# Optimization experiments

Hardware: AMD Instinct MI355X
Metric: run time of the kernel (lower is better)

## Reference

```python
import jax, jax.numpy as jnp
import numpy as np

B, S, SE = 4, 1024, 1024
E, H, M = 768, 12, 100
D = E // H
EPS = 1e-5
GELU_C = 0.7978845608028654  # sqrt(2/pi)


def _ln(x, g, b):
    mu = x.mean(-1, keepdims=True)
    v = ((x - mu) ** 2).mean(-1, keepdims=True)
    return g * (x - mu) / jnp.sqrt(v + EPS) + b


def _gelu(x):
    return 0.5 * x * (1.0 + jnp.tanh(GELU_C * (x + 0.044715 * x ** 3)))


def _split(x):  # [b,s,E] -> [b,H,s,D]
    b, s, _ = x.shape
    return x.reshape(b, s, H, D).transpose(0, 2, 1, 3)


def _merge(x):  # [b,H,s,D] -> [b,s,E]
    b, h, s, d = x.shape
    return x.transpose(0, 2, 1, 3).reshape(b, s, h * d)


def _forward(x, encoder_features, ln1_g, ln1_b, ln2_g, ln2_b,
             c_attn_w, c_attn_b, attn_proj_w, attn_proj_b,
             memory_features, mem_attn_w, mem_attn_b, mem_alpha_w, mem_alpha_b,
             fcq_w, fcq_b, fck_w, fck_b, fcv_w, fcv_b, enc_proj_w, enc_proj_b,
             fc_alpha1_w, fc_alpha1_b, fc_alpha2_w, fc_alpha2_b,
             mlp_fc_w, mlp_fc_b, mlp_proj_w, mlp_proj_b, mask_encoder):
    # ---- memory-augmented self-attention (note: original has NO 1/sqrt(d) scaling here) ----
    h = _ln(x, ln1_g, ln1_b)
    qkv = h @ c_attn_w + c_attn_b
    q, k, v = jnp.split(qkv, 3, axis=-1)
    q, k, v = _split(q), _split(k), _split(v)
    w = jax.nn.softmax(jnp.einsum('bhqd,bhkd->bhqk', q, k), axis=-1)
    a = _merge(jnp.einsum('bhqk,bhkd->bhqd', w, v))
    # memory slots are batch-independent -> compute once, broadcast over batch
    mem = memory_features[0] @ mem_attn_w + mem_attn_b  # [M, 2E]
    mk, mv = jnp.split(mem, 2, axis=-1)
    mk = mk.reshape(M, H, D).transpose(1, 2, 0)  # [H,D,M]
    mv = mv.reshape(M, H, D).transpose(1, 0, 2)  # [H,M,D]
    wm = jax.nn.softmax(jnp.einsum('bhqd,hdm->bhqm', q, mk), axis=-1)
    a1 = _merge(jnp.einsum('bhqm,hmd->bhqd', wm, mv))
    al = jax.nn.sigmoid(jnp.concatenate([a, a1], -1) @ mem_alpha_w + mem_alpha_b)
    a = al * a + (1.0 - al) * a1
    a = a @ attn_proj_w + attn_proj_b
    a = x + a  # residual (dropout = identity in eval)

    # ---- two cross-attentions sharing weights and ln_1 ----
    ha = _ln(a, ln1_g, ln1_b)

    def enc_dec(enc):
        qe = _split(ha @ fcq_w + fcq_b)
        ke = _split(enc @ fck_w + fck_b)
        ve = _split(enc @ fcv_w + fcv_b)
        we = jnp.einsum('bhqd,bhkd->bhqk', qe, ke) / np.float32(np.sqrt(D))
        we = jnp.where(mask_encoder, jnp.float32(-10000.0), we)
        we = jax.nn.softmax(we, axis=-1)
        o = _merge(jnp.einsum('bhqk,bhkd->bhqd', we, ve))
        return o @ enc_proj_w + enc_proj_b

    e1 = enc_dec(_ln(encoder_features[:, 0], ln1_g, ln1_b))
    e2 = enc_dec(_ln(encoder_features[:, 1], ln1_g, ln1_b))
    al1 = jax.nn.sigmoid(jnp.concatenate([a, e1], -1) @ fc_alpha1_w + fc_alpha1_b)
    al2 = jax.nn.sigmoid(jnp.concatenate([a, e2], -1) @ fc_alpha2_w + fc_alpha2_b)
    e1 = al1 * a + (1.0 - al1) * e1
    e2 = al2 * a + (1.0 - al2) * e2
    a = (e1 + e2) / np.float32(np.sqrt(2.0))

    # ---- MLP ----
    hm = _ln(a, ln2_g, ln2_b)
    m = _gelu(hm @ mlp_fc_w + mlp_fc_b) @ mlp_proj_w + mlp_proj_b
    return a + m


def setup_inputs() -> dict:
    key = jax.random.key(0)
    ks = iter(jax.random.split(key, 48))

    def rn(shape, s=0.02):
        return jax.random.normal(next(ks), shape, jnp.float32) * s

    return dict(
        x=jax.random.normal(next(ks), (B, S, E), jnp.float32),
        encoder_features=jax.random.normal(next(ks), (B, 2, SE, E), jnp.float32),
        mask_encoder=jax.random.bernoulli(next(ks), 0.1, (B, 1, 1, SE)),
        ln1_g=jnp.ones(E, jnp.float32), ln1_b=jnp.zeros(E, jnp.float32),
        ln2_g=jnp.ones(E, jnp.float32), ln2_b=jnp.zeros(E, jnp.float32),
        c_attn_w=rn((E, 3 * E)), c_attn_b=jnp.zeros(3 * E, jnp.float32),
        attn_proj_w=rn((E, E)), attn_proj_b=jnp.zeros(E, jnp.float32),
        memory_features=rn((1, M, E), 1.0),
        mem_attn_w=rn((E, 2 * E)), mem_attn_b=jnp.zeros(2 * E, jnp.float32),
        mem_alpha_w=rn((2 * E, E)), mem_alpha_b=jnp.zeros(E, jnp.float32),
        fcq_w=rn((E, E)), fcq_b=jnp.zeros(E, jnp.float32),
        fck_w=rn((E, E)), fck_b=jnp.zeros(E, jnp.float32),
        fcv_w=rn((E, E)), fcv_b=jnp.zeros(E, jnp.float32),
        enc_proj_w=rn((E, E)), enc_proj_b=jnp.zeros(E, jnp.float32),
        fc_alpha1_w=rn((2 * E, E)), fc_alpha1_b=jnp.zeros(E, jnp.float32),
        fc_alpha2_w=rn((2 * E, E)), fc_alpha2_b=jnp.zeros(E, jnp.float32),
        mlp_fc_w=rn((E, 4 * E)), mlp_fc_b=jnp.zeros(4 * E, jnp.float32),
        mlp_proj_w=rn((4 * E, E)), mlp_proj_b=jnp.zeros(E, jnp.float32),
    )


def reference(x, encoder_features, mask_encoder, ln1_g, ln1_b, ln2_g, ln2_b,
              c_attn_w, c_attn_b, attn_proj_w, attn_proj_b,
              memory_features, mem_attn_w, mem_attn_b, mem_alpha_w, mem_alpha_b,
              fcq_w, fcq_b, fck_w, fck_b, fcv_w, fcv_b, enc_proj_w, enc_proj_b,
              fc_alpha1_w, fc_alpha1_b, fc_alpha2_w, fc_alpha2_b,
              mlp_fc_w, mlp_fc_b, mlp_proj_w, mlp_proj_b):
    return _forward(x, encoder_features, ln1_g, ln1_b, ln2_g, ln2_b,
                    c_attn_w, c_attn_b, attn_proj_w, attn_proj_b,
                    memory_features, mem_attn_w, mem_attn_b, mem_alpha_w, mem_alpha_b,
                    fcq_w, fcq_b, fck_w, fck_b, fcv_w, fcv_b, enc_proj_w, enc_proj_b,
                    fc_alpha1_w, fc_alpha1_b, fc_alpha2_w, fc_alpha2_b,
                    mlp_fc_w, mlp_fc_b, mlp_proj_w, mlp_proj_b, mask_encoder)
```

## Files before the change

kernel.cpp:

```cpp
#include <hip/hip_runtime.h>

typedef __bf16 bf16_t;
typedef __bf16 bf16x8v __attribute__((ext_vector_type(8)));
typedef float f32x4 __attribute__((ext_vector_type(4)));

#define CB 4
#define CE 768
#define CH 12
#define CD 64

__device__ __forceinline__ float fexp2(float x) { return __builtin_amdgcn_exp2f(x); }

__device__ __forceinline__ void gload16(const void* g, void* l) {
    __builtin_amdgcn_global_load_lds((const __attribute__((address_space(1))) void*)g,
                                     (__attribute__((address_space(3))) void*)l, 16, 0, 0);
}

__device__ __forceinline__ void xcd_remap(int& bx, int& by, int gx, int gy) {
    int nwg = gx * gy;
    if ((nwg & 7) == 0) {
        int lin = by * gx + bx;
        int lin2 = (lin & 7) * (nwg >> 3) + (lin >> 3);
        bx = lin2 % gx;
        by = lin2 / gx;
    }
}

template<int BM, int BN, int CONCAT, int ACT, int RES, int OUT, int CMODE>
__global__ __launch_bounds__(256)
void gemm_n(const bf16_t* __restrict__ A0, const bf16_t* __restrict__ A1,
            const bf16_t* __restrict__ Bt, const float* __restrict__ bias,
            const float* __restrict__ bias2, const void* __restrict__ resid,
            void* __restrict__ C, void* __restrict__ C2, void* __restrict__ C3,
            int M, int N, int K, int lda, int ldc)
{
    constexpr int WM = BM / 2, WN = BN / 2, RM = WM / 16, RN = WN / 16;
    __shared__ __align__(16) bf16_t As0[BM * 64], As1[BM * 64];
    __shared__ __align__(16) bf16_t Bs0[BN * 64], Bs1[BN * 64];

    const int t = threadIdx.x;
    const int lane = t & 63, wave = t >> 6;
    int bx = blockIdx.x, by = blockIdx.y;
    xcd_remap(bx, by, gridDim.x, gridDim.y);
    const int m0 = by * BM, n0 = bx * BN;
    const int wm = (wave & 1) * WM, wn = (wave >> 1) * WN;
    const int fr = lane & 15, quad = lane >> 4;

    const int lr = lane >> 3;
    const int kof = ((lane & 7) ^ lr) * 8;

    const bf16_t* A1b = A1;
    if (CMODE == 6) A1b = A1 + (n0 >= 768 ? (long)4096 * 768 : 0);

    f32x4 acc[RM][RN];
#pragma unroll
    for (int i = 0; i < RM; i++)
#pragma unroll
        for (int j = 0; j < RN; j++)
#pragma unroll
            for (int p = 0; p < 4; p++) acc[i][j][p] = 0.f;

    auto stage = [&](bf16_t* As, bf16_t* Bs, int kt) {
        const bf16_t* Ab = A0;
        int kk = kt;
        if (CONCAT && kt >= 768) { Ab = A1b; kk = kt - 768; }
        const bf16_t* asrc = Ab + (long)(m0 + wave * 8 + lr) * lda + kk + kof;
#pragma unroll
        for (int c = 0; c < BM / 32; ++c)
            gload16(asrc + (long)c * 32 * lda, &As[(c * 32 + wave * 8) * 64]);
        const bf16_t* bsrc = Bt + (long)(n0 + wave * 8 + lr) * K + kt + kof;
#pragma unroll
        for (int c = 0; c < BN / 32; ++c)
            gload16(bsrc + (long)c * 32 * K, &Bs[(c * 32 + wave * 8) * 64]);
    };

    const int sw = fr & 7;
    auto compute = [&](const bf16_t* As, const bf16_t* Bs) {
        bf16x8v af[RM][2], bfr[RN][2];
        const int s0 = quad ^ sw;
#pragma unroll
        for (int i = 0; i < RM; ++i) {
            const char* rb = (const char*)As + (wm + i * 16 + fr) * 128;
            af[i][0] = *(const bf16x8v*)(rb + (s0 << 4));
            af[i][1] = *(const bf16x8v*)(rb + ((s0 ^ 4) << 4));
        }
#pragma unroll
        for (int j = 0; j < RN; ++j) {
            const char* rb = (const char*)Bs + (wn + j * 16 + fr) * 128;
            bfr[j][0] = *(const bf16x8v*)(rb + (s0 << 4));
            bfr[j][1] = *(const bf16x8v*)(rb + ((s0 ^ 4) << 4));
        }
#pragma unroll
        for (int ks = 0; ks < 2; ++ks)
#pragma unroll
            for (int i = 0; i < RM; ++i)
#pragma unroll
                for (int j = 0; j < RN; ++j)
                    acc[i][j] = __builtin_amdgcn_mfma_f32_16x16x32_bf16(af[i][ks], bfr[j][ks], acc[i][j], 0, 0, 0);
    };

    const int nk = K >> 6;
    stage(As0, Bs0, 0);
    __syncthreads();
    for (int kt = 0; kt + 2 <= nk; kt += 2) {
        stage(As1, Bs1, (kt + 1) << 6);
        compute(As0, Bs0);
        __syncthreads();
        if (kt + 2 < nk) stage(As0, Bs0, (kt + 2) << 6);
        compute(As1, Bs1);
        __syncthreads();
    }

    const int rq = quad * 4, cn = fr;
#pragma unroll
    for (int i = 0; i < RM; i++)
#pragma unroll
        for (int j = 0; j < RN; j++) {
            int col = n0 + wn + j * 16 + cn;
            int t3 = (CMODE == 4 || CMODE == 5) ? (col / 768) : 0;
            int cc = col - t3 * 768;
            float bv = 0.f;
            if (CMODE == 5)      bv = t3 ? bias2[cc] : bias[cc];
            else if (CMODE == 6) bv = (col < 768) ? bias[col] : bias2[col - 768];
            else if (bias)       bv = bias[col];
            const int row0 = m0 + wm + i * 16 + rq;
            float vv[4];
#pragma unroll
            for (int p = 0; p < 4; p++) {
                float v = acc[i][j][p] + bv;
                if (ACT == 1) v = 1.f / (1.f + __expf(-v));
                if (ACT == 2) {
                    float u2 = 1.5957691216057308f * (v + 0.044715f * v * v * v);
                    v = v / (1.f + __expf(-u2));
                }
                if (RES == 2) v += ((const float*)resid)[(long)(row0 + p) * ldc + col];
                vv[p] = v;
            }
            if (CMODE == 0) {
#pragma unroll
                for (int p = 0; p < 4; p++) {
                    long idx = (long)(row0 + p) * ldc + col;
                    if (OUT == 0)      ((bf16_t*)C)[idx] = (bf16_t)vv[p];
                    else if (OUT == 1) ((float*)C)[idx] = vv[p];
                    else { ((float*)C)[idx] = vv[p]; ((bf16_t*)C2)[idx] = (bf16_t)vv[p]; }
                }
            } else if (CMODE == 6) {
                long base = (col < 768) ? 0 : ((long)4096 * 768 - 768);
#pragma unroll
                for (int p = 0; p < 4; p++)
                    ((bf16_t*)C)[base + (long)(row0 + p) * 768 + col] = (bf16_t)vv[p];
            } else if (CMODE == 7) {
#pragma unroll
                for (int p = 0; p < 4; p++) {
                    long idx = (long)(row0 + p) * ldc + col;
                    float a  = (float)((const bf16_t*)C2)[idx];
                    float a1 = (float)((const bf16_t*)C3)[idx];
                    ((bf16_t*)C)[idx] = (bf16_t)(vv[p] * a + (1.f - vv[p]) * a1);
                }
            } else {
                int bb = row0 >> 10, ss0 = row0 & 1023;
                int hh = cc >> 6, dd = cc & 63;
                long srow = (long)(bb * CH + hh) * 1024 + ss0;
                long tbase = (((long)(bb * CH + hh) * 64) + dd) * 1024 + ss0;
                union { ushort4 u4; bf16_t b[4]; } pk;
#pragma unroll
                for (int p = 0; p < 4; p++) pk.b[p] = (bf16_t)vv[p];
                if (CMODE == 2) {
#pragma unroll
                    for (int p = 0; p < 4; p++)
                        ((bf16_t*)C)[(srow + p) * 64 + dd] = pk.b[p];
                } else if (CMODE == 5) {
                    if (t3 == 0) {
#pragma unroll
                        for (int p = 0; p < 4; p++)
                            ((bf16_t*)C)[(srow + p) * 64 + dd] = pk.b[p];
                    } else {
                        *(ushort4*)((bf16_t*)C2 + tbase) = pk.u4;
                    }
                } else {
                    if (t3 == 0) {
#pragma unroll
                        for (int p = 0; p < 4; p++)
                            ((bf16_t*)C)[(srow + p) * 64 + dd] = pk.b[p];
                    } else if (t3 == 1) {
#pragma unroll
                        for (int p = 0; p < 4; p++)
                            ((bf16_t*)C2)[(srow + p) * 64 + dd] = pk.b[p];
                    } else {
                        *(ushort4*)((bf16_t*)C3 + tbase) = pk.u4;
                    }
                }
            }
        }
}

template<int MODE, int QR>
__global__ __launch_bounds__(256)
void flash_attn(const bf16_t* __restrict__ Q, const bf16_t* __restrict__ K,
                const bf16_t* __restrict__ V, const int* __restrict__ mask,
                bf16_t* __restrict__ O)
{
    constexpr int QG = QR / 64;
    __shared__ __align__(16) bf16_t Qs[QR * 64];
    __shared__ __align__(16) bf16_t Ks0[64 * 64], Ks1[64 * 64];
    __shared__ __align__(16) bf16_t Vs[64 * 64];

    const int t = threadIdx.x;
    const int lane = t & 63, wave = t >> 6;
    int bx = blockIdx.x, bz = blockIdx.z;
    {
        int nwg = gridDim.x * gridDim.z;
        if ((nwg & 7) == 0) {
            int lin = bz * gridDim.x + bx;
            int lin2 = (lin & 7) * (nwg >> 3) + (lin >> 3);
            bx = lin2 % gridDim.x;
            bz = lin2 / gridDim.x;
        }
    }
    const int zq = (MODE == 1) ? (bz % 48) : bz;
    const int b = zq / CH, h = bz % CH;
    const long eoff = (MODE == 1) ? (long)(bz / 48) * ((long)4096 * 768) : 0;
    const int q0 = bx * QR;

    const bf16_t* Qb = Q + (long)zq * 65536 + (long)q0 * 64;
    const bf16_t* Kb = (MODE == 2) ? K + (long)h * (128 * 64) : K + (long)bz * 65536;
    const bf16_t* Vb = (MODE == 2) ? V + (long)h * (64 * 128) : V + (long)bz * 65536;
    const int ldv = (MODE == 2) ? 128 : 1024;
    const int NT = (MODE == 2) ? 2 : 16;
    constexpr float SCL = (MODE == 1) ? 0.18033688011112042f : 1.4426950408889634f;

    const int lr = lane >> 3, kof = ((lane & 7) ^ lr) * 8;

    auto stageK = [&](bf16_t* Ks, int kt) {
#pragma unroll
        for (int c = 0; c < 2; ++c) {
            int r = wave * 8 + c * 32;
            gload16(Kb + (long)(kt * 64 + r + lr) * 64 + kof, &Ks[r * 64]);
        }
    };
    auto stageV = [&](int kt) {
#pragma unroll
        for (int c = 0; c < 2; ++c) {
            int r = wave * 8 + c * 32;
            gload16(Vb + (long)(r + lr) * ldv + kt * 64 + kof, &Vs[r * 64]);
        }
    };

    stageK(Ks0, 0);
#pragma unroll
    for (int c = 0; c < QR / 32; ++c) {
        int r = wave * 8 + c * 32;
        gload16(Qb + (long)(r + lr) * 64 + kof, &Qs[r * 64]);
    }
    __syncthreads();

    const int fr = lane & 15, quad = lane >> 4;
    const int sw = fr & 7;
    bf16x8v qf[QG][2];
#pragma unroll
    for (int g = 0; g < QG; g++)
#pragma unroll
        for (int ks = 0; ks < 2; ks++) {
            const char* rb = (const char*)Qs + (wave * (16 * QG) + g * 16 + fr) * 128;
            bf16x8v raw = *(const bf16x8v*)(rb + (((quad ^ sw) ^ (ks << 2)) << 4));
#pragma unroll
            for (int i = 0; i < 8; i++) qf[g][ks][i] = (bf16_t)((float)raw[i] * SCL);
        }

    bf16_t* Ps = &Qs[wave * (16 * QG) * 64];

    f32x4 o[4][QG];
    float mrow[QG], lrow[QG];
#pragma unroll
    for (int g = 0; g < QG; g++) { mrow[g] = -1e30f; lrow[g] = 0.f; }
#pragma unroll
    for (int j = 0; j < 4; j++)
#pragma unroll
        for (int g = 0; g < QG; g++)
#pragma unroll
            for (int p = 0; p < 4; p++) o[j][g][p] = 0.f;

    auto qkt_sm = [&](const bf16_t* Ks, int kt) {
        f32x4 s[4][QG];
#pragma unroll
        for (int j = 0; j < 4; j++)
#pragma unroll
            for (int g = 0; g < QG; g++)
#pragma unroll
                for (int p = 0; p < 4; p++) s[j][g][p] = 0.f;
        __builtin_amdgcn_s_setprio(1);
#pragma unroll
        for (int ks = 0; ks < 2; ks++) {
            bf16x8v bk[4];
#pragma unroll
            for (int j = 0; j < 4; j++) {
                const char* rb = (const char*)Ks + (j * 16 + fr) * 128;
                bk[j] = *(const bf16x8v*)(rb + (((quad ^ sw) ^ (ks << 2)) << 4));
            }
#pragma unroll
            for (int j = 0; j < 4; j++)
#pragma unroll
                for (int g = 0; g < QG; g++)
                    s[j][g] = __builtin_amdgcn_mfma_f32_16x16x32_bf16(bk[j], qf[g][ks], s[j][g], 0, 0, 0);
        }
        __builtin_amdgcn_s_setprio(0);
        if (MODE == 1) {
#pragma unroll
            for (int j = 0; j < 4; j++) {
                int4 mv = *(const int4*)&mask[(long)b * 1024 + kt * 64 + j * 16 + quad * 4];
#pragma unroll
                for (int g = 0; g < QG; g++) {
                    s[j][g][0] = mv.x ? -14426.95f : s[j][g][0];
                    s[j][g][1] = mv.y ? -14426.95f : s[j][g][1];
                    s[j][g][2] = mv.z ? -14426.95f : s[j][g][2];
                    s[j][g][3] = mv.w ? -14426.95f : s[j][g][3];
                }
            }
        }
        if (MODE == 2) {
#pragma unroll
            for (int j = 0; j < 4; j++)
#pragma unroll
                for (int p = 0; p < 4; p++)
                    if (kt * 64 + j * 16 + quad * 4 + p >= 100)
#pragma unroll
                        for (int g = 0; g < QG; g++) s[j][g][p] = -1e30f;
        }
        float tmax[QG];
        bool need = false;
#pragma unroll
        for (int g = 0; g < QG; g++) {
            float tm = s[0][g][0];
#pragma unroll
            for (int j = 0; j < 4; j++)
#pragma unroll
                for (int p = 0; p < 4; p++) tm = fmaxf(tm, s[j][g][p]);
            tm = fmaxf(tm, __shfl_xor(tm, 16, 64));
            tm = fmaxf(tm, __shfl_xor(tm, 32, 64));
            tmax[g] = tm;
            need = need || (tm > mrow[g] + 8.f);
        }
        if (__any(need ? 1 : 0)) {
#pragma unroll
            for (int g = 0; g < QG; g++) {
                float mnew = fmaxf(mrow[g], tmax[g]);
                float alpha = fexp2(mrow[g] - mnew);
                lrow[g] *= alpha;
                mrow[g] = mnew;
                float arow[4];
#pragma unroll
                for (int p = 0; p < 4; p++)
                    arow[p] = __shfl(alpha, (lane & 48) | (quad * 4 + p), 64);
#pragma unroll
                for (int j = 0; j < 4; j++)
#pragma unroll
                    for (int p = 0; p < 4; p++) o[j][g][p] *= arow[p];
            }
        }
#pragma unroll
        for (int g = 0; g < QG; g++) {
            float rs = 0.f;
#pragma unroll
            for (int j = 0; j < 4; j++)
#pragma unroll
                for (int p = 0; p < 4; p++) {
                    float e = fexp2(s[j][g][p] - mrow[g]);
                    s[j][g][p] = e;
                    rs += e;
                }
            rs += __shfl_xor(rs, 16, 64);
            rs += __shfl_xor(rs, 32, 64);
            lrow[g] += rs;
        }
#pragma unroll
        for (int j = 0; j < 4; j++)
#pragma unroll
            for (int g = 0; g < QG; g++) {
                union { uint2 u; bf16_t bb[4]; } pk;
#pragma unroll
                for (int p = 0; p < 4; p++) pk.bb[p] = (bf16_t)s[j][g][p];
                int row = g * 16 + fr;
                *(uint2*)((char*)Ps + row * 128 +
                          (((j * 2 + (quad >> 1)) ^ sw) << 4) + ((quad & 1) << 3)) = pk.u;
            }
    };

    auto pv = [&]() {
        __builtin_amdgcn_s_setprio(1);
#pragma unroll
        for (int ks = 0; ks < 2; ks++) {
            bf16x8v af[QG], bv[4];
#pragma unroll
            for (int g = 0; g < QG; g++) {
                const char* rb = (const char*)Ps + (g * 16 + fr) * 128;
                af[g] = *(const bf16x8v*)(rb + (((quad ^ sw) ^ (ks << 2)) << 4));
            }
#pragma unroll
            for (int j = 0; j < 4; j++) {
                const char* rb = (const char*)Vs + (j * 16 + fr) * 128;
                bv[j] = *(const bf16x8v*)(rb + (((quad ^ sw) ^ (ks << 2)) << 4));
            }
#pragma unroll
            for (int j = 0; j < 4; j++)
#pragma unroll
                for (int g = 0; g < QG; g++)
                    o[j][g] = __builtin_amdgcn_mfma_f32_16x16x32_bf16(af[g], bv[j], o[j][g], 0, 0, 0);
        }
        __builtin_amdgcn_s_setprio(0);
    };

    for (int kt = 0; kt < NT; kt += 2) {
        stageV(kt);
        if (kt + 1 < NT) stageK(Ks1, kt + 1);
        qkt_sm(Ks0, kt);
        __syncthreads();
        pv();
        __syncthreads();
        stageV(kt + 1);
        if (kt + 2 < NT) stageK(Ks0, kt + 2);
        qkt_sm(Ks1, kt + 1);
        __syncthreads();
        pv();
        __syncthreads();
    }
#pragma unroll
    for (int g = 0; g < QG; g++) {
        float linv[4];
#pragma unroll
        for (int p = 0; p < 4; p++)
            linv[p] = 1.f / __shfl(lrow[g], (lane & 48) | (quad * 4 + p), 64);
#pragma unroll
        for (int p = 0; p < 4; p++) {
            int srow = q0 + wave * (16 * QG) + g * 16 + quad * 4 + p;
            long base = ((long)b * 1024 + srow) * 768 + h * 64 + eoff;
#pragma unroll
            for (int j = 0; j < 4; j++)
                O[base + j * 16 + fr] = (bf16_t)(o[j][g][p] * linv[p]);
        }
    }
}

__device__ __forceinline__ void ln_body(const float* in, bf16_t* out,
                                        const float* g, const float* b,
                                        long base, long ob, int t)
{
    __shared__ float red[4];
    float v0 = in[base + t], v1 = in[base + t + 256], v2 = in[base + t + 512];
    float s = v0 + v1 + v2;
    for (int m = 32; m; m >>= 1) s += __shfl_xor(s, m, 64);
    if ((t & 63) == 0) red[t >> 6] = s;
    __syncthreads();
    s = red[0] + red[1] + red[2] + red[3];
    __syncthreads();
    const float mu = s * (1.f / 768.f);
    float d0 = v0 - mu, d1 = v1 - mu, d2 = v2 - mu;
    float q = d0 * d0 + d1 * d1 + d2 * d2;
    for (int m = 32; m; m >>= 1) q += __shfl_xor(q, m, 64);
    if ((t & 63) == 0) red[t >> 6] = q;
    __syncthreads();
    q = red[0] + red[1] + red[2] + red[3];
    const float rstd = rsqrtf(q * (1.f / 768.f) + 1e-5f);
    out[ob + t]       = (bf16_t)(g[t]       * d0 * rstd + b[t]);
    out[ob + t + 256] = (bf16_t)(g[t + 256] * d1 * rstd + b[t + 256]);
    out[ob + t + 512] = (bf16_t)(g[t + 512] * d2 * rstd + b[t + 512]);
}

__global__ __launch_bounds__(256)
void ln_kernel(const float* __restrict__ in, bf16_t* __restrict__ out,
               const float* __restrict__ g, const float* __restrict__ b)
{
    const int r = blockIdx.x;
    ln_body(in, out, g, b, (long)r * CE, (long)r * CE, threadIdx.x);
}

__global__ __launch_bounds__(256)
void ln_enc(const float* __restrict__ encf, bf16_t* __restrict__ out,
            const float* __restrict__ g, const float* __restrict__ b)
{
    const int r = blockIdx.x;
    const int e = r >> 12, rr = r & 4095, bb = rr >> 10, s = rr & 1023;
    ln_body(encf, out, g, b, ((long)(bb * 2 + e) * 1024 + s) * CE, (long)r * CE, threadIdx.x);
}

__global__ void fuse_gates2(const bf16_t* __restrict__ gal, const bf16_t* __restrict__ eo,
                            float* __restrict__ rf)
{
    const long SZel = (long)4096 * 768;
    long idx = (long)blockIdx.x * 256 + threadIdx.x;
    float g1 = (float)gal[idx], g2 = (float)gal[idx + SZel];
    float e1 = (float)eo[idx],  e2 = (float)eo[idx + SZel];
    float r = rf[idx];
    float v = g1 * r + (1.f - g1) * e1 + g2 * r + (1.f - g2) * e2;
    rf[idx] = v * 0.7071067811865476f;
}

__global__ void zero_out(float* __restrict__ out)
{
    out[blockIdx.x * 256 + threadIdx.x] = 0.f;
}

__global__ void transpose_cast(const float* __restrict__ in, bf16_t* __restrict__ out,
                               int K, int N)
{
    __shared__ bf16_t tile[32][33];
    int n0 = blockIdx.x * 32, k0 = blockIdx.y * 32;
    int tx = threadIdx.x, ty = threadIdx.y;
    for (int i = ty; i < 32; i += 8)
        tile[i][tx] = (bf16_t)in[(long)(k0 + i) * N + n0 + tx];
    __syncthreads();
    for (int i = ty; i < 32; i += 8)
        out[(long)(n0 + i) * K + k0 + tx] = tile[tx][i];
}

__global__ void cast_pad_mem(const float* __restrict__ memf, bf16_t* __restrict__ out)
{
    int idx = blockIdx.x * 256 + threadIdx.x;
    int row = idx / 768;
    out[idx] = (row < 100) ? (bf16_t)memf[idx] : (bf16_t)0.f;
}

__global__ void repack_mem(const bf16_t* __restrict__ mem, bf16_t* __restrict__ mkt,
                           bf16_t* __restrict__ mvt)
{
    int idx = blockIdx.x * 256 + threadIdx.x;
    int d = idx & 63;
    int slot = (idx >> 6) & 127;
    int h = idx >> 13;
    bf16_t kv = (slot < 100) ? mem[slot * 1536 + h * CD + d] : (bf16_t)0.f;
    bf16_t vv = (slot < 100) ? mem[slot * 1536 + CE + h * CD + d] : (bf16_t)0.f;
    mkt[idx] = kv;
    mvt[((long)h * 64 + d) * 128 + slot] = vv;
}

extern "C" void kernel_launch(void* const* d_in, const int* in_sizes, int n_in,
                              void* d_out, int out_size, void* d_ws, size_t ws_size,
                              hipStream_t stream)
{
    (void)in_sizes; (void)n_in; (void)out_size;
    const float* x        = (const float*)d_in[0];
    const float* encf     = (const float*)d_in[1];
    const int*   maskenc  = (const int*)d_in[2];
    const float* ln1_g    = (const float*)d_in[3];
    const float* ln1_b    = (const float*)d_in[4];
    const float* ln2_g    = (const float*)d_in[5];
    const float* ln2_b    = (const float*)d_in[6];
    const float* c_attn_w = (const float*)d_in[7];
    const float* c_attn_b = (const float*)d_in[8];
    const float* aproj_w  = (const float*)d_in[9];
    const float* aproj_b  = (const float*)d_in[10];
    const float* memf     = (const float*)d_in[11];
    const float* mattn_w  = (const float*)d_in[12];
    const float* mattn_b  = (const float*)d_in[13];
    const float* malpha_w = (const float*)d_in[14];
    const float* malpha_b = (const float*)d_in[15];
    const float* fcq_w    = (const float*)d_in[16];
    const float* fcq_b    = (const float*)d_in[17];
    const float* fck_w    = (const float*)d_in[18];
    const float* fck_b    = (const float*)d_in[19];
    const float* fcv_w    = (const float*)d_in[20];
    const float* fcv_b    = (const float*)d_in[21];
    const float* eproj_w  = (const float*)d_in[22];
    const float* eproj_b  = (const float*)d_in[23];
    const float* fa1_w    = (const float*)d_in[24];
    const float* fa1_b    = (const float*)d_in[25];
    const float* fa2_w    = (const float*)d_in[26];
    const float* fa2_b    = (const float*)d_in[27];
    const float* mfc_w    = (const float*)d_in[28];
    const float* mfc_b    = (const float*)d_in[29];
    const float* mproj_w  = (const float*)d_in[30];
    const float* mproj_b  = (const float*)d_in[31];
    float* dout = (float*)d_out;

    size_t off = 0;
    auto alloc = [&](size_t bytes) -> void* {
        void* p = (char*)d_ws + off;
        off = (off + bytes + 255) & ~(size_t)255;
        return p;
    };
    const size_t SZ = (size_t)4096 * 768 * 2;
    const long SZel = (long)4096 * 768;
    bf16_t* wt_cattn  = (bf16_t*)alloc((size_t)2304 * 768 * 2);
    bf16_t* wt_aproj  = (bf16_t*)alloc((size_t)768 * 768 * 2);
    bf16_t* wt_malpha = (bf16_t*)alloc((size_t)768 * 1536 * 2);
    bf16_t* wt_fcq    = (bf16_t*)alloc((size_t)768 * 768 * 2);
    bf16_t* wt_fck    = (bf16_t*)alloc((size_t)768 * 768 * 2);
    bf16_t* wt_fcv    = (bf16_t*)alloc((size_t)768 * 768 * 2);
    bf16_t* wt_eproj  = (bf16_t*)alloc((size_t)768 * 768 * 2);
    bf16_t* wt_fa1    = (bf16_t*)alloc((size_t)768 * 1536 * 2);
    bf16_t* wt_fa2    = (bf16_t*)alloc((size_t)768 * 1536 * 2);
    bf16_t* wt_mfc    = (bf16_t*)alloc((size_t)3072 * 768 * 2);
    bf16_t* wt_mproj  = (bf16_t*)alloc((size_t)768 * 3072 * 2);
    bf16_t* wt_mattn  = (bf16_t*)alloc((size_t)1536 * 768 * 2);
    bf16_t* memb   = (bf16_t*)alloc((size_t)128 * 768 * 2);
    bf16_t* membuf = (bf16_t*)alloc((size_t)128 * 1536 * 2);
    bf16_t* mkt    = (bf16_t*)alloc((size_t)CH * 128 * 64 * 2);
    bf16_t* mvt    = (bf16_t*)alloc((size_t)CH * 64 * 128 * 2);
    bf16_t* bufA   = (bf16_t*)alloc(SZ);
    bf16_t* qbuf   = (bf16_t*)alloc(SZ);
    bf16_t* kbuf   = (bf16_t*)alloc(2 * SZ);
    bf16_t* vtbuf  = (bf16_t*)alloc(2 * SZ);
    bf16_t* asbuf  = (bf16_t*)alloc(2 * SZ);
    bf16_t* bufB   = (bf16_t*)alloc(2 * SZ);
    float*  residf = (float*)alloc((size_t)4096 * 768 * 4);
    bf16_t* residb = (bf16_t*)alloc(SZ);

    if (off > ws_size) {
        zero_out<<<12288, 256, 0, stream>>>(dout);
        return;
    }
    bf16_t* mid = kbuf;
    bf16_t* galbuf = kbuf;
    bf16_t* eobuf = bufB;

    const dim3 blk(256);

    auto T = [&](const float* w, bf16_t* wt, int Kd, int Nd) {
        transpose_cast<<<dim3(Nd / 32, Kd / 32), dim3(32, 8), 0, stream>>>(w, wt, Kd, Nd);
    };
    T(c_attn_w, wt_cattn, 768, 2304);
    T(aproj_w, wt_aproj, 768, 768);
    T(malpha_w, wt_malpha, 1536, 768);
    T(fcq_w, wt_fcq, 768, 768);
    T(fck_w, wt_fck, 768, 768);
    T(fcv_w, wt_fcv, 768, 768);
    T(eproj_w, wt_eproj, 768, 768);
    T(fa1_w, wt_fa1, 1536, 768);
    T(fa2_w, wt_fa2, 1536, 768);
    T(mfc_w, wt_mfc, 768, 3072);
    T(mproj_w, wt_mproj, 3072, 768);
    T(mattn_w, wt_mattn, 768, 1536);

    cast_pad_mem<<<384, blk, 0, stream>>>(memf, memb);
    gemm_n<64,64,0,0,0,0,0><<<dim3(24, 2), blk, 0, stream>>>(
        memb, nullptr, wt_mattn, mattn_b, nullptr, nullptr, membuf, nullptr, nullptr,
        128, 1536, 768, 768, 1536);
    repack_mem<<<384, blk, 0, stream>>>(membuf, mkt, mvt);

    ln_kernel<<<4096, blk, 0, stream>>>(x, bufA, ln1_g, ln1_b);
    gemm_n<128,128,0,0,0,0,4><<<dim3(18, 32), blk, 0, stream>>>(
        bufA, nullptr, wt_cattn, c_attn_b, nullptr, nullptr, qbuf, kbuf, vtbuf,
        4096, 2304, 768, 768, 0);

    flash_attn<0,64><<<dim3(16, 1, 48), blk, 0, stream>>>(qbuf, kbuf, vtbuf, nullptr, asbuf);
    flash_attn<2,64><<<dim3(16, 1, 48), blk, 0, stream>>>(qbuf, mkt, mvt, nullptr, asbuf + SZel);

    gemm_n<128,64,1,1,0,0,7><<<dim3(12, 32), blk, 0, stream>>>(
        asbuf, asbuf + SZel, wt_malpha, malpha_b, nullptr, nullptr, bufA, asbuf, asbuf + SZel,
        4096, 768, 1536, 768, 768);
    gemm_n<128,64,0,0,2,2,0><<<dim3(12, 32), blk, 0, stream>>>(
        bufA, nullptr, wt_aproj, aproj_b, nullptr, x, residf, residb, nullptr,
        4096, 768, 768, 768, 768);

    ln_kernel<<<4096, blk, 0, stream>>>(residf, bufA, ln1_g, ln1_b);
    gemm_n<128,64,0,0,0,0,2><<<dim3(12, 32), blk, 0, stream>>>(
        bufA, nullptr, wt_fcq, fcq_b, nullptr, nullptr, qbuf, nullptr, nullptr,
        4096, 768, 768, 768, 0);

    ln_enc<<<8192, blk, 0, stream>>>(encf, bufB, ln1_g, ln1_b);
    gemm_n<128,128,0,0,0,0,5><<<dim3(12, 64), blk, 0, stream>>>(
        bufB, nullptr, wt_fck, fck_b, fcv_b, nullptr, kbuf, vtbuf, nullptr,
        8192, 1536, 768, 768, 0);
    flash_attn<1,128><<<dim3(8, 1, 96), blk, 0, stream>>>(
        qbuf, kbuf, vtbuf, maskenc, asbuf);
    gemm_n<128,128,0,0,0,0,0><<<dim3(6, 64), blk, 0, stream>>>(
        asbuf, nullptr, wt_eproj, eproj_b, nullptr, nullptr, eobuf, nullptr, nullptr,
        8192, 768, 768, 768, 768);
    gemm_n<128,64,1,1,0,0,6><<<dim3(24, 32), blk, 0, stream>>>(
        residb, eobuf, wt_fa1, fa1_b, fa2_b, nullptr, galbuf, nullptr, nullptr,
        4096, 1536, 1536, 768, 768);
    fuse_gates2<<<12288, blk, 0, stream>>>(galbuf, eobuf, residf);

    ln_kernel<<<4096, blk, 0, stream>>>(residf, bufA, ln2_g, ln2_b);
    gemm_n<128,128,0,2,0,0,0><<<dim3(24, 32), blk, 0, stream>>>(
        bufA, nullptr, wt_mfc, mfc_b, nullptr, nullptr, mid, nullptr, nullptr,
        4096, 3072, 768, 768, 3072);
    gemm_n<128,64,0,0,2,1,0><<<dim3(12, 32), blk, 0, stream>>>(
        mid, nullptr, wt_mproj, mproj_b, nullptr, residf, dout, nullptr, nullptr,
        4096, 768, 3072, 3072, 768);
}
```

Before: 593.4 us.

## Batch weight transposes into one launch and shrink GEMM tiles for more workgroups

All twelve weight transpose-casts now run in a single kernel launch. Each block finds its weight matrix through a prefix-sum table passed as a kernel argument. Separately, several GEMMs move from 128x128 or 128x64 tiles to 128x64 or 64x64 tiles with matching grids, so more workgroups cover the 256 CUs of the MI355X. This trades more total operand reloads and less reuse per tile for better load balance and less launch overhead.

```diff
diff --git a/kernel.cpp b/kernel.cpp
--- a/kernel.cpp
+++ b/kernel.cpp
@@ -499,11 +499,27 @@
     out[blockIdx.x * 256 + threadIdx.x] = 0.f;
 }
 
-__global__ void transpose_cast(const float* __restrict__ in, bf16_t* __restrict__ out,
-                               int K, int N)
+#define NTW 12
+struct TTab {
+    const float* src[NTW];
+    unsigned long dst[NTW];
+    int kn[NTW];
+    int pre[NTW + 1];
+};
+
+__global__ void transpose_all(TTab tt, char* __restrict__ ws)
 {
     __shared__ bf16_t tile[32][33];
-    int n0 = blockIdx.x * 32, k0 = blockIdx.y * 32;
+    int tb = blockIdx.x;
+    int e = 0;
+#pragma unroll
+    for (int i = 0; i < NTW; i++) if (tb >= tt.pre[i + 1]) e = i + 1;
+    int local = tb - tt.pre[e];
+    const int K = tt.kn[e] >> 16, N = tt.kn[e] & 0xffff;
+    const float* in = tt.src[e];
+    bf16_t* out = (bf16_t*)(ws + tt.dst[e]);
+    const int ntx = N / 32;
+    const int n0 = (local % ntx) * 32, k0 = (local / ntx) * 32;
     int tx = threadIdx.x, ty = threadIdx.y;
     for (int i = ty; i < 32; i += 8)
         tile[i][tx] = (bf16_t)in[(long)(k0 + i) * N + n0 + tx];
@@ -614,21 +630,25 @@
 
     const dim3 blk(256);
 
-    auto T = [&](const float* w, bf16_t* wt, int Kd, int Nd) {
-        transpose_cast<<<dim3(Nd / 32, Kd / 32), dim3(32, 8), 0, stream>>>(w, wt, Kd, Nd);
-    };
-    T(c_attn_w, wt_cattn, 768, 2304);
-    T(aproj_w, wt_aproj, 768, 768);
-    T(malpha_w, wt_malpha, 1536, 768);
-    T(fcq_w, wt_fcq, 768, 768);
-    T(fck_w, wt_fck, 768, 768);
-    T(fcv_w, wt_fcv, 768, 768);
-    T(eproj_w, wt_eproj, 768, 768);
-    T(fa1_w, wt_fa1, 1536, 768);
-    T(fa2_w, wt_fa2, 1536, 768);
-    T(mfc_w, wt_mfc, 768, 3072);
-    T(mproj_w, wt_mproj, 3072, 768);
-    T(mattn_w, wt_mattn, 768, 1536);
+    TTab tt;
+    {
+        const float* srcs[NTW] = {c_attn_w, aproj_w, malpha_w, fcq_w, fck_w, fcv_w,
+                                  eproj_w, fa1_w, fa2_w, mfc_w, mproj_w, mattn_w};
+        bf16_t* dsts[NTW] = {wt_cattn, wt_aproj, wt_malpha, wt_fcq, wt_fck, wt_fcv,
+                             wt_eproj, wt_fa1, wt_fa2, wt_mfc, wt_mproj, wt_mattn};
+        int Ks[NTW] = {768, 768, 1536, 768, 768, 768, 768, 1536, 1536, 768, 3072, 768};
+        int Ns[NTW] = {2304, 768, 768, 768, 768, 768, 768, 768, 768, 3072, 768, 1536};
+        int acc = 0;
+        for (int i = 0; i < NTW; i++) {
+            tt.src[i] = srcs[i];
+            tt.dst[i] = (unsigned long)((char*)dsts[i] - (char*)d_ws);
+            tt.kn[i] = (Ks[i] << 16) | Ns[i];
+            tt.pre[i] = acc;
+            acc += (Ks[i] / 32) * (Ns[i] / 32);
+        }
+        tt.pre[NTW] = acc;
+        transpose_all<<<acc, dim3(32, 8), 0, stream>>>(tt, (char*)d_ws);
+    }
 
     cast_pad_mem<<<384, blk, 0, stream>>>(memf, memb);
     gemm_n<64,64,0,0,0,0,0><<<dim3(24, 2), blk, 0, stream>>>(
@@ -637,32 +657,32 @@
     repack_mem<<<384, blk, 0, stream>>>(membuf, mkt, mvt);
 
     ln_kernel<<<4096, blk, 0, stream>>>(x, bufA, ln1_g, ln1_b);
-    gemm_n<128,128,0,0,0,0,4><<<dim3(18, 32), blk, 0, stream>>>(
+    gemm_n<128,64,0,0,0,0,4><<<dim3(36, 32), blk, 0, stream>>>(
         bufA, nullptr, wt_cattn, c_attn_b, nullptr, nullptr, qbuf, kbuf, vtbuf,
         4096, 2304, 768, 768, 0);
 
     flash_attn<0,64><<<dim3(16, 1, 48), blk, 0, stream>>>(qbuf, kbuf, vtbuf, nullptr, asbuf);
     flash_attn<2,64><<<dim3(16, 1, 48), blk, 0, stream>>>(qbuf, mkt, mvt, nullptr, asbuf + SZel);
 
-    gemm_n<128,64,1,1,0,0,7><<<dim3(12, 32), blk, 0, stream>>>(
+    gemm_n<64,64,1,1,0,0,7><<<dim3(12, 64), blk, 0, stream>>>(
         asbuf, asbuf + SZel, wt_malpha, malpha_b, nullptr, nullptr, bufA, asbuf, asbuf + SZel,
         4096, 768, 1536, 768, 768);
-    gemm_n<128,64,0,0,2,2,0><<<dim3(12, 32), blk, 0, stream>>>(
+    gemm_n<64,64,0,0,2,2,0><<<dim3(12, 64), blk, 0, stream>>>(
         bufA, nullptr, wt_aproj, aproj_b, nullptr, x, residf, residb, nullptr,
         4096, 768, 768, 768, 768);
 
     ln_kernel<<<4096, blk, 0, stream>>>(residf, bufA, ln1_g, ln1_b);
-    gemm_n<128,64,0,0,0,0,2><<<dim3(12, 32), blk, 0, stream>>>(
+    gemm_n<64,64,0,0,0,0,2><<<dim3(12, 64), blk, 0, stream>>>(
         bufA, nullptr, wt_fcq, fcq_b, nullptr, nullptr, qbuf, nullptr, nullptr,
         4096, 768, 768, 768, 0);
 
     ln_enc<<<8192, blk, 0, stream>>>(encf, bufB, ln1_g, ln1_b);
-    gemm_n<128,128,0,0,0,0,5><<<dim3(12, 64), blk, 0, stream>>>(
+    gemm_n<128,64,0,0,0,0,5><<<dim3(24, 64), blk, 0, stream>>>(
         bufB, nullptr, wt_fck, fck_b, fcv_b, nullptr, kbuf, vtbuf, nullptr,
         8192, 1536, 768, 768, 0);
     flash_attn<1,128><<<dim3(8, 1, 96), blk, 0, stream>>>(
         qbuf, kbuf, vtbuf, maskenc, asbuf);
-    gemm_n<128,128,0,0,0,0,0><<<dim3(6, 64), blk, 0, stream>>>(
+    gemm_n<128,64,0,0,0,0,0><<<dim3(12, 64), blk, 0, stream>>>(
         asbuf, nullptr, wt_eproj, eproj_b, nullptr, nullptr, eobuf, nullptr, nullptr,
         8192, 768, 768, 768, 768);
     gemm_n<128,64,1,1,0,0,6><<<dim3(24, 32), blk, 0, stream>>>(
@@ -671,7 +691,7 @@
     fuse_gates2<<<12288, blk, 0, stream>>>(galbuf, eobuf, residf);
 
     ln_kernel<<<4096, blk, 0, stream>>>(residf, bufA, ln2_g, ln2_b);
-    gemm_n<128,128,0,2,0,0,0><<<dim3(24, 32), blk, 0, stream>>>(
+    gemm_n<128,64,0,2,0,0,0><<<dim3(48, 32), blk, 0, stream>>>(
         bufA, nullptr, wt_mfc, mfc_b, nullptr, nullptr, mid, nullptr, nullptr,
         4096, 3072, 768, 768, 3072);
     gemm_n<128,64,0,0,2,1,0><<<dim3(12, 32), blk, 0, stream>>>(
```

Measured after the change: 541.1 us. 1.1x faster.
